# Kernel optimization log

Hardware: AMD Instinct MI355X
Metric: run time of the kernel (lower is better)

Reference implementation:

```python
import jax, jax.numpy as jnp
import numpy as np

B, L, D_IN, H, C = 64, 2048, 400, 200, 32
NEG = 1e12


def setup_inputs() -> dict:
    key = jax.random.key(0)
    k1, k2, k3, k4, k5 = jax.random.split(key, 5)
    x = jax.random.normal(k1, (B, L, D_IN), dtype=jnp.float32)
    category_bias = jax.random.normal(k2, (B, L, C), dtype=jnp.float32)
    att_mask = (jax.random.uniform(k3, (B, L)) > 0.2).astype(jnp.float32)
    # glorot-uniform-ish scales
    W_proj = jax.random.normal(k4, (D_IN, H), dtype=jnp.float32) * np.float32(np.sqrt(2.0 / (D_IN + H)))
    context = jax.random.normal(k5, (C, H), dtype=jnp.float32) * np.float32(np.sqrt(2.0 / (C + H)))
    lamada = jnp.zeros((1,), dtype=jnp.float32)
    return {"x": x, "category_bias": category_bias, "att_mask": att_mask,
            "W_proj": W_proj, "context": context, "lamada": lamada}


def reference(x, category_bias, att_mask, W_proj, context, lamada):
    # proj: [B, L, H] = tanh(x @ W_proj)  (Dense, no bias)
    proj = jnp.tanh(jnp.einsum("bld,dh->blh", x, W_proj))
    # scores vs learned context vectors: [B, L, C]
    weights = jnp.einsum("blh,ch->blc", proj, context) + lamada * category_bias
    # [B, C, L]
    weights = jnp.transpose(weights, (0, 2, 1))
    # additive large-negative mask, then softmax over sequence
    weights = weights - (1.0 - att_mask[:, None, :]) * NEG
    weights = jax.nn.softmax(weights, axis=-1)
    # poly representation: [B, C, D_IN]
    return jnp.einsum("bcl,bld->bcd", weights, x)
```

## Files before the change

### kernel.cpp

```cpp
#include <hip/hip_runtime.h>
#include <cmath>
#include <cstdint>

#define B_ 64
#define L_ 2048
#define DIN 400
#define H_ 200
#define C_ 32
#define NEGBIG 1e12f
#define KC1 13
#define NT1 13
#define KC2 7
#define MT2 2
#define NLC 8

typedef _Float16 half8 __attribute__((ext_vector_type(8)));
typedef float f32x4 __attribute__((ext_vector_type(4)));
typedef unsigned int uint4v __attribute__((ext_vector_type(4)));

__device__ __align__(16) _Float16 g_wfrag[KC1 * NT1 * 512];
__device__ __align__(16) _Float16 g_cfrag[KC2 * MT2 * 512];

static __device__ __forceinline__ f32x4 mfma16(half8 a, half8 b, f32x4 c) {
  return __builtin_amdgcn_mfma_f32_16x16x32_f16(a, b, c, 0, 0, 0);
}

static __device__ __forceinline__ float fast_tanh(float v) {
  const float e = __expf(2.0f * v);
  return 1.0f - 2.0f / (e + 1.0f);
}

__global__ __launch_bounds__(64) void k_prep(const float* __restrict__ Wp,
                                             const float* __restrict__ ctx)
{
  const int lane = threadIdx.x;
  const int bid = blockIdx.x;
  if (bid < KC1 * NT1) {
    const int q = bid / NT1, nt = bid % NT1;
    const int kb = q * 32 + (lane >> 4) * 8;
    const int n  = nt * 16 + (lane & 15);
    half8 h;
#pragma unroll
    for (int j = 0; j < 8; ++j) {
      const int k = kb + j;
      const float v = (k < DIN && n < H_) ? Wp[(size_t)k * H_ + n] : 0.0f;
      h[j] = (_Float16)v;
    }
    *reinterpret_cast<half8*>(&g_wfrag[((size_t)bid << 9) + (lane << 3)]) = h;
  } else {
    const int r = bid - KC1 * NT1;
    const int c  = (r % MT2) * 16 + (lane & 15);
    const int hb = (r / MT2) * 32 + (lane >> 4) * 8;
    half8 h;
#pragma unroll
    for (int j = 0; j < 8; ++j) {
      const int hh = hb + j;
      const float v = (hh < H_) ? ctx[(size_t)c * H_ + hh] : 0.0f;
      h[j] = (_Float16)v;
    }
    *reinterpret_cast<half8*>(&g_cfrag[((size_t)r << 9) + (lane << 3)]) = h;
  }
}

__global__ __launch_bounds__(256, 4) void k_scores(
    const float* __restrict__ x,
    const float* __restrict__ cb,
    const float* __restrict__ mask,
    const float* __restrict__ lam,
    float* __restrict__ S)
{
  __shared__ half8 smemv[1792];

  const int tid  = threadIdx.x;
  const int lane = tid & 63;
  const int w    = __builtin_amdgcn_readfirstlane(tid >> 6);
  const int b    = blockIdx.y;
  const int l0   = blockIdx.x * 64;
  const int oct  = lane >> 4;

  f32x4 acc[NT1];
#pragma unroll
  for (int nt = 0; nt < NT1; ++nt) acc[nt] = f32x4{0.f, 0.f, 0.f, 0.f};

  const float* xrow =
      x + ((size_t)b * L_ + l0 + w * 16 + (lane & 15)) * DIN + oct * 8;

  for (int i = w; i < NT1; i += 4) {
    const _Float16* gp = g_wfrag + (((size_t)i) << 9) + (lane << 3);
    __builtin_amdgcn_global_load_lds(
        (const __attribute__((address_space(1))) void*)gp,
        (__attribute__((address_space(3))) void*)(smemv + i * 64),
        16, 0, 0);
  }
  __builtin_amdgcn_sched_barrier(0);
  float4 cur0 = *reinterpret_cast<const float4*>(xrow);
  float4 cur1 = *reinterpret_cast<const float4*>(xrow + 4);

#pragma unroll
  for (int q = 0; q < KC1; ++q) {
    asm volatile("s_waitcnt vmcnt(2)\n\ts_barrier" ::: "memory");

    float4 nx0 = float4{0.f, 0.f, 0.f, 0.f};
    float4 nx1 = float4{0.f, 0.f, 0.f, 0.f};
    if (q < KC1 - 1) {
      const int nb = ((q + 1) & 1) * 832;
      for (int i = w; i < NT1; i += 4) {
        const _Float16* gp =
            g_wfrag + (((size_t)((q + 1) * NT1 + i)) << 9) + (lane << 3);
        __builtin_amdgcn_global_load_lds(
            (const __attribute__((address_space(1))) void*)gp,
            (__attribute__((address_space(3))) void*)(smemv + nb + i * 64),
            16, 0, 0);
      }
      __builtin_amdgcn_sched_barrier(0);
      const int k0 = (q + 1) * 32 + oct * 8;
      if (k0 + 7 < DIN) {
        nx0 = *reinterpret_cast<const float4*>(xrow + (q + 1) * 32);
        nx1 = *reinterpret_cast<const float4*>(xrow + (q + 1) * 32 + 4);
      }
    }

    float fa[8] = {cur0.x, cur0.y, cur0.z, cur0.w,
                   cur1.x, cur1.y, cur1.z, cur1.w};
    half8 ah;
#pragma unroll
    for (int j = 0; j < 8; ++j) ah[j] = (_Float16)fa[j];

    const int base = (q & 1) * 832;
#pragma unroll
    for (int nt = 0; nt < NT1; ++nt) {
      const half8 bh = smemv[base + nt * 64 + lane];
      acc[nt] = mfma16(ah, bh, acc[nt]);
    }
    cur0 = nx0;
    cur1 = nx1;
  }

  __syncthreads();
  if (lane >= 32) {
    half8 z = {};
    smemv[(24 + w) * 64 + lane] = z;
  }
  _Float16* Pp = reinterpret_cast<_Float16*>(smemv);
#pragma unroll
  for (int nt = 0; nt < NT1; ++nt) {
    const int h   = nt * 16 + (lane & 15);
    const int q2  = h >> 5;
    const int lpw = ((h >> 3) & 3) << 4;
    const int jj  = h & 7;
#pragma unroll
    for (int reg = 0; reg < 4; ++reg) {
      const int t = ((lane >> 4) << 2) + reg;
      const float p = fast_tanh(acc[nt][reg]);
      Pp[(size_t)(((q2 * 4 + w) * 64) + lpw + t) * 8 + jj] = (_Float16)p;
    }
  }

  f32x4 s0 = f32x4{0.f, 0.f, 0.f, 0.f};
  f32x4 s1 = f32x4{0.f, 0.f, 0.f, 0.f};
#pragma unroll
  for (int q2 = 0; q2 < KC2; ++q2) {
    const half8 pb = smemv[(q2 * 4 + w) * 64 + lane];
    const half8 c0 = *reinterpret_cast<const half8*>(
        g_cfrag + (((size_t)(q2 * 2)) << 9) + (lane << 3));
    const half8 c1 = *reinterpret_cast<const half8*>(
        g_cfrag + (((size_t)(q2 * 2 + 1)) << 9) + (lane << 3));
    s0 = mfma16(c0, pb, s0);
    s1 = mfma16(c1, pb, s1);
  }

  const int tok = (w << 4) | (lane & 15);
  const size_t bl = (size_t)b * L_ + l0 + tok;
  const float lamv = lam[0];
  const float mk = (1.0f - mask[bl]) * NEGBIG;
  const int cq = (lane >> 4) << 2;
  const float4 cb0 = *reinterpret_cast<const float4*>(cb + bl * C_ + cq);
  const float4 cb1 = *reinterpret_cast<const float4*>(cb + bl * C_ + 16 + cq);
  float* Sp = S + (size_t)b * C_ * L_ + l0 + tok;
  Sp[(size_t)(cq + 0) * L_] = s0[0] + lamv * cb0.x - mk;
  Sp[(size_t)(cq + 1) * L_] = s0[1] + lamv * cb0.y - mk;
  Sp[(size_t)(cq + 2) * L_] = s0[2] + lamv * cb0.z - mk;
  Sp[(size_t)(cq + 3) * L_] = s0[3] + lamv * cb0.w - mk;
  Sp[(size_t)(16 + cq + 0) * L_] = s1[0] + lamv * cb1.x - mk;
  Sp[(size_t)(16 + cq + 1) * L_] = s1[1] + lamv * cb1.y - mk;
  Sp[(size_t)(16 + cq + 2) * L_] = s1[2] + lamv * cb1.z - mk;
  Sp[(size_t)(16 + cq + 3) * L_] = s1[3] + lamv * cb1.w - mk;
}

__global__ __launch_bounds__(256) void k_softmax(float* __restrict__ S,
                                                 _Float16* __restrict__ wh)
{
  const int row = blockIdx.x;
  float* R = S + (size_t)row * L_;
  const int tid = threadIdx.x;

  float v[8];
  float m = -3.4e38f;
#pragma unroll
  for (int j = 0; j < 8; ++j) {
    v[j] = R[tid + 256 * j];
    m = fmaxf(m, v[j]);
  }
#pragma unroll
  for (int o = 32; o > 0; o >>= 1) m = fmaxf(m, __shfl_xor(m, o));

  __shared__ float red[4];
  const int wid = tid >> 6;
  if ((tid & 63) == 0) red[wid] = m;
  __syncthreads();
  m = fmaxf(fmaxf(red[0], red[1]), fmaxf(red[2], red[3]));
  __syncthreads();

  float s = 0.f;
#pragma unroll
  for (int j = 0; j < 8; ++j) {
    v[j] = __expf(v[j] - m);
    s += v[j];
  }
#pragma unroll
  for (int o = 32; o > 0; o >>= 1) s += __shfl_xor(s, o);
  if ((tid & 63) == 0) red[wid] = s;
  __syncthreads();
  s = red[0] + red[1] + red[2] + red[3];

  const float inv = 1.0f / s;
  if (wh != nullptr) {
    _Float16* whr = wh + (size_t)row * L_;
#pragma unroll
    for (int j = 0; j < 8; ++j)
      whr[tid + 256 * j] = (_Float16)(v[j] * inv);
  } else {
#pragma unroll
    for (int j = 0; j < 8; ++j) R[tid + 256 * j] = v[j] * inv;
  }
}

__global__ __launch_bounds__(512, 4) void k_out_mfma(
    const float* __restrict__ x,
    const _Float16* __restrict__ wh,
    float* __restrict__ part)
{
  __shared__ unsigned int xsw[400 * 20];
  __shared__ unsigned int ws16[32][16];

  const int tid  = threadIdx.x;
  const int lane = tid & 63;
  const int w    = __builtin_amdgcn_readfirstlane(tid >> 6);
  const int b    = blockIdx.y;
  const int kq   = blockIdx.x;
  const int l0b  = kq * (L_ / NLC);

  const int ntile0 = (w < 7) ? w * 3 : 21;
  const int NTW    = (w < 7) ? 3 : 4;

  const int n   = lane & 15;
  const int oct = lane >> 4;

  f32x4 acc[4][2];
#pragma unroll
  for (int i = 0; i < 4; ++i) {
    acc[i][0] = f32x4{0.f, 0.f, 0.f, 0.f};
    acc[i][1] = f32x4{0.f, 0.f, 0.f, 0.f};
  }

  const float* xb = x + ((size_t)b * L_ + l0b) * DIN;
  const unsigned int* whb = reinterpret_cast<const unsigned int*>(
      wh + (size_t)b * C_ * L_ + l0b);

  float4 r0[4], r1[4];
  unsigned int wreg;

#pragma unroll
  for (int s = 0; s < 4; ++s) {
    const int i = s * 512 + tid;
    if (s < 3 || i < 1600) {
      const int lp = i / 100, qd = i - lp * 100;
      const float* src = xb + (size_t)(2 * lp) * DIN + 4 * qd;
      r0[s] = *reinterpret_cast<const float4*>(src);
      r1[s] = *reinterpret_cast<const float4*>(src + DIN);
    }
  }
  wreg = whb[((size_t)(tid >> 4) * L_) / 2 + (tid & 15)];

  const int NCH = (L_ / NLC) / 32;
  for (int ch = 0; ch < NCH; ++ch) {
    __syncthreads();

#pragma unroll
    for (int s = 0; s < 4; ++s) {
      const int i = s * 512 + tid;
      if (s < 3 || i < 1600) {
        const int lp = i / 100, qd = i - lp * 100;
#pragma unroll
        for (int k = 0; k < 4; ++k) {
          const int d = 4 * qd + k;
          const int sw = ((d >> 2) ^ (d >> 4)) & 3;
          const int col = (((lp >> 2) ^ sw) << 2) | (lp & 3);
          const _Float16 h0 = (_Float16)r0[s][k];
          const _Float16 h1 = (_Float16)r1[s][k];
          unsigned int pk = (unsigned int)__builtin_bit_cast(unsigned short, h0) |
                            ((unsigned int)__builtin_bit_cast(unsigned short, h1) << 16);
          xsw[d * 20 + col] = pk;
        }
      }
    }
    ws16[tid >> 4][tid & 15] = wreg;
    __syncthreads();

    if (ch + 1 < NCH) {
      const float* xc = xb + (size_t)((ch + 1) * 32) * DIN;
#pragma unroll
      for (int s = 0; s < 4; ++s) {
        const int i = s * 512 + tid;
        if (s < 3 || i < 1600) {
          const int lp = i / 100, qd = i - lp * 100;
          const float* src = xc + (size_t)(2 * lp) * DIN + 4 * qd;
          r0[s] = *reinterpret_cast<const float4*>(src);
          r1[s] = *reinterpret_cast<const float4*>(src + DIN);
        }
      }
      wreg = whb[((size_t)(tid >> 4) * L_ + (ch + 1) * 32) / 2 + (tid & 15)];
    }

    union { uint4v u; half8 h; } a0c, a1c;
    a0c.u = *reinterpret_cast<const uint4v*>(&ws16[n][oct * 4]);
    a1c.u = *reinterpret_cast<const uint4v*>(&ws16[n + 16][oct * 4]);
    const half8 a0 = a0c.h;
    const half8 a1 = a1c.h;

#pragma unroll
    for (int nt = 0; nt < 4; ++nt) {
      if (nt < NTW) {
        const int d0 = (ntile0 + nt) * 16 + n;
        const int sw = ((d0 >> 2) ^ (d0 >> 4)) & 3;
        const half8 bh = *reinterpret_cast<const half8*>(
            &xsw[d0 * 20 + ((oct ^ sw) << 2)]);
        acc[nt][0] = mfma16(a0, bh, acc[nt][0]);
        acc[nt][1] = mfma16(a1, bh, acc[nt][1]);
      }
    }
  }

  float* pb = part + ((size_t)(b * NLC + kq) * C_) * DIN;
#pragma unroll
  for (int nt = 0; nt < 4; ++nt) {
    if (nt < NTW) {
      const int d = (ntile0 + nt) * 16 + n;
#pragma unroll
      for (int mt = 0; mt < 2; ++mt) {
#pragma unroll
        for (int reg = 0; reg < 4; ++reg) {
          const int c = mt * 16 + oct * 4 + reg;
          pb[(size_t)c * DIN + d] = acc[nt][mt][reg];
        }
      }
    }
  }
}

__global__ __launch_bounds__(256) void k_out_reduce(
    const float* __restrict__ part, float* __restrict__ out)
{
  const int idx = blockIdx.x * 256 + threadIdx.x;
  const int b = idx / (C_ * DIN / 4);
  const int r = idx - b * (C_ * DIN / 4);
  const float4* p = reinterpret_cast<const float4*>(part) +
                    (size_t)b * NLC * (C_ * DIN / 4) + r;
  float4 s = float4{0.f, 0.f, 0.f, 0.f};
#pragma unroll
  for (int lc = 0; lc < NLC; ++lc) {
    const float4 v = p[(size_t)lc * (C_ * DIN / 4)];
    s.x += v.x; s.y += v.y; s.z += v.z; s.w += v.w;
  }
  reinterpret_cast<float4*>(out)[idx] = s;
}

__global__ __launch_bounds__(256) void k_out_atomic(
    const float* __restrict__ x,
    const float* __restrict__ Wt,
    float* __restrict__ out)
{
  __shared__ float ws_s[C_][256];
  const int tid  = threadIdx.x;
  const int b    = blockIdx.y;
  const int lc0  = blockIdx.x * 256;
  const int g    = __builtin_amdgcn_readfirstlane(tid >> 6);
  const int lane = tid & 63;

  {
    const int c  = tid >> 3;
    const int lb = (tid & 7) * 32;
    const float* src = Wt + ((size_t)b * C_ + c) * L_ + lc0 + lb;
#pragma unroll
    for (int j = 0; j < 32; j += 4)
      *reinterpret_cast<float4*>(&ws_s[c][lb + j]) =
          *reinterpret_cast<const float4*>(src + j);
  }
  __syncthreads();

  float a1[8][4] = {};
  float a2[8][4] = {};
  const bool has2 = lane < 36;
  const float* xb = x + ((size_t)b * L_ + lc0) * DIN;
  const int d1 = lane * 4;
  const int d2 = 256 + lane * 4;

  for (int l = 0; l < 256; ++l) {
    const float4 xv = *reinterpret_cast<const float4*>(xb + (size_t)l * DIN + d1);
    float4 xv2 = float4{0.f, 0.f, 0.f, 0.f};
    if (has2) xv2 = *reinterpret_cast<const float4*>(xb + (size_t)l * DIN + d2);
#pragma unroll
    for (int i = 0; i < 8; ++i) {
      const float wv = ws_s[g * 8 + i][l];
      a1[i][0] = fmaf(wv, xv.x, a1[i][0]);
      a1[i][1] = fmaf(wv, xv.y, a1[i][1]);
      a1[i][2] = fmaf(wv, xv.z, a1[i][2]);
      a1[i][3] = fmaf(wv, xv.w, a1[i][3]);
      a2[i][0] = fmaf(wv, xv2.x, a2[i][0]);
      a2[i][1] = fmaf(wv, xv2.y, a2[i][1]);
      a2[i][2] = fmaf(wv, xv2.z, a2[i][2]);
      a2[i][3] = fmaf(wv, xv2.w, a2[i][3]);
    }
  }

  float* ob = out + ((size_t)b * C_ + g * 8) * DIN;
#pragma unroll
  for (int i = 0; i < 8; ++i) {
#pragma unroll
    for (int kk = 0; kk < 4; ++kk)
      atomicAdd(ob + (size_t)i * DIN + d1 + kk, a1[i][kk]);
    if (has2) {
#pragma unroll
      for (int kk = 0; kk < 4; ++kk)
        atomicAdd(ob + (size_t)i * DIN + d2 + kk, a2[i][kk]);
    }
  }
}

extern "C" void kernel_launch(void* const* d_in, const int* in_sizes, int n_in,
                              void* d_out, int out_size, void* d_ws, size_t ws_size,
                              hipStream_t stream)
{
  const float* x    = (const float*)d_in[0];
  const float* cb   = (const float*)d_in[1];
  const float* mask = (const float*)d_in[2];
  const float* Wp   = (const float*)d_in[3];
  const float* ctx  = (const float*)d_in[4];
  const float* lam  = (const float*)d_in[5];
  float* out = (float*)d_out;

  const size_t part_elems = (size_t)B_ * NLC * C_ * DIN;
  float* wsf  = (float*)d_ws;
  float* S    = wsf;
  float* part = wsf;
  _Float16* wh = (_Float16*)(wsf + part_elems);
  const size_t need = part_elems * sizeof(float) +
                      (size_t)B_ * C_ * L_ * sizeof(_Float16);

  k_prep<<<dim3(KC1 * NT1 + KC2 * MT2), 64, 0, stream>>>(Wp, ctx);
  k_scores<<<dim3(L_ / 64, B_), 256, 0, stream>>>(x, cb, mask, lam, S);

  if (ws_size >= need) {
    k_softmax<<<dim3(B_ * C_), 256, 0, stream>>>(S, wh);
    k_out_mfma<<<dim3(NLC, B_), 512, 0, stream>>>(x, wh, part);
    k_out_reduce<<<dim3(B_ * C_ * DIN / 4 / 256), 256, 0, stream>>>(part, out);
  } else {
    k_softmax<<<dim3(B_ * C_), 256, 0, stream>>>(S, nullptr);
    hipMemsetAsync(d_out, 0, (size_t)out_size * sizeof(float), stream);
    k_out_atomic<<<dim3(L_ / 256, B_), 256, 0, stream>>>(x, S, out);
  }
}
```

Before: 107.0 us.

## Switch score projection GEMM to 32x32x16 MFMA with 2x2 wave tiling

Rewrites the projection GEMM in k_scores to use 32x32x16 f16 MFMA. Waves are arranged as 2 M-tiles by 2 N-halves instead of each wave owning 16 rows across all 13 N-tiles. The W fragment layout in k_prep is rebuilt to match, and the tanh write-back into LDS is remapped for the 32x32 accumulator layout. The goal is fewer MFMA issues and fewer LDS B-fragment reads per FLOP. The trade-offs are higher accumulator register use (launch bounds drop from 4 to 3 blocks), an extra barrier, and uneven work between waves (4 vs 3 N-tiles).

```diff
diff --git a/kernel.cpp b/kernel.cpp
--- a/kernel.cpp
+++ b/kernel.cpp
@@ -8,21 +8,26 @@
 #define H_ 200
 #define C_ 32
 #define NEGBIG 1e12f
-#define KC1 13
-#define NT1 13
+#define KI1 13
+#define KT1 26
+#define NW1 7
 #define KC2 7
 #define MT2 2
 #define NLC 8
 
 typedef _Float16 half8 __attribute__((ext_vector_type(8)));
 typedef float f32x4 __attribute__((ext_vector_type(4)));
+typedef float f32x16 __attribute__((ext_vector_type(16)));
 typedef unsigned int uint4v __attribute__((ext_vector_type(4)));
 
-__device__ __align__(16) _Float16 g_wfrag[KC1 * NT1 * 512];
+__device__ __align__(16) _Float16 g_wfrag[KT1 * NW1 * 512];
 __device__ __align__(16) _Float16 g_cfrag[KC2 * MT2 * 512];
 
 static __device__ __forceinline__ f32x4 mfma16(half8 a, half8 b, f32x4 c) {
   return __builtin_amdgcn_mfma_f32_16x16x32_f16(a, b, c, 0, 0, 0);
+}
+static __device__ __forceinline__ f32x16 mfma32(half8 a, half8 b, f32x16 c) {
+  return __builtin_amdgcn_mfma_f32_32x32x16_f16(a, b, c, 0, 0, 0);
 }
 
 static __device__ __forceinline__ float fast_tanh(float v) {
@@ -35,10 +40,10 @@
 {
   const int lane = threadIdx.x;
   const int bid = blockIdx.x;
-  if (bid < KC1 * NT1) {
-    const int q = bid / NT1, nt = bid % NT1;
-    const int kb = q * 32 + (lane >> 4) * 8;
-    const int n  = nt * 16 + (lane & 15);
+  if (bid < KT1 * NW1) {
+    const int kt = bid / NW1, nt = bid % NW1;
+    const int kb = kt * 16 + (lane >> 5) * 8;
+    const int n  = nt * 32 + (lane & 31);
     half8 h;
 #pragma unroll
     for (int j = 0; j < 8; ++j) {
@@ -48,7 +53,7 @@
     }
     *reinterpret_cast<half8*>(&g_wfrag[((size_t)bid << 9) + (lane << 3)]) = h;
   } else {
-    const int r = bid - KC1 * NT1;
+    const int r = bid - KT1 * NW1;
     const int c  = (r % MT2) * 16 + (lane & 15);
     const int hb = (r / MT2) * 32 + (lane >> 4) * 8;
     half8 h;
@@ -62,7 +67,7 @@
   }
 }
 
-__global__ __launch_bounds__(256, 4) void k_scores(
+__global__ __launch_bounds__(256, 3) void k_scores(
     const float* __restrict__ x,
     const float* __restrict__ cb,
     const float* __restrict__ mask,
@@ -74,18 +79,21 @@
   const int tid  = threadIdx.x;
   const int lane = tid & 63;
   const int w    = __builtin_amdgcn_readfirstlane(tid >> 6);
+  const int mtile = w & 1;
+  const int nh    = w >> 1;
+  const int nt0   = nh * 4;
+  const int NTWV  = nh ? 3 : 4;
   const int b    = blockIdx.y;
   const int l0   = blockIdx.x * 64;
-  const int oct  = lane >> 4;
-
-  f32x4 acc[NT1];
-#pragma unroll
-  for (int nt = 0; nt < NT1; ++nt) acc[nt] = f32x4{0.f, 0.f, 0.f, 0.f};
+
+  f32x16 acc[4];
+#pragma unroll
+  for (int i = 0; i < 4; ++i) acc[i] = f32x16{};
 
   const float* xrow =
-      x + ((size_t)b * L_ + l0 + w * 16 + (lane & 15)) * DIN + oct * 8;
-
-  for (int i = w; i < NT1; i += 4) {
+      x + ((size_t)b * L_ + l0 + mtile * 32 + (lane & 31)) * DIN + (lane >> 5) * 8;
+
+  for (int i = w; i < 14; i += 4) {
     const _Float16* gp = g_wfrag + (((size_t)i) << 9) + (lane << 3);
     __builtin_amdgcn_global_load_lds(
         (const __attribute__((address_space(1))) void*)gp,
@@ -93,68 +101,90 @@
         16, 0, 0);
   }
   __builtin_amdgcn_sched_barrier(0);
-  float4 cur0 = *reinterpret_cast<const float4*>(xrow);
-  float4 cur1 = *reinterpret_cast<const float4*>(xrow + 4);
-
-#pragma unroll
-  for (int q = 0; q < KC1; ++q) {
-    asm volatile("s_waitcnt vmcnt(2)\n\ts_barrier" ::: "memory");
-
-    float4 nx0 = float4{0.f, 0.f, 0.f, 0.f};
-    float4 nx1 = float4{0.f, 0.f, 0.f, 0.f};
-    if (q < KC1 - 1) {
-      const int nb = ((q + 1) & 1) * 832;
-      for (int i = w; i < NT1; i += 4) {
+  float4 cur[2][2];
+#pragma unroll
+  for (int s = 0; s < 2; ++s) {
+    cur[s][0] = *reinterpret_cast<const float4*>(xrow + s * 16);
+    cur[s][1] = *reinterpret_cast<const float4*>(xrow + s * 16 + 4);
+  }
+
+#pragma unroll
+  for (int q = 0; q < KI1; ++q) {
+    asm volatile("s_waitcnt vmcnt(4)\n\ts_barrier" ::: "memory");
+
+    float4 nx[2][2];
+#pragma unroll
+    for (int s = 0; s < 2; ++s) {
+      nx[s][0] = float4{0.f, 0.f, 0.f, 0.f};
+      nx[s][1] = float4{0.f, 0.f, 0.f, 0.f};
+    }
+    if (q < KI1 - 1) {
+      const int nb = ((q + 1) & 1) * 896;
+      for (int i = w; i < 14; i += 4) {
         const _Float16* gp =
-            g_wfrag + (((size_t)((q + 1) * NT1 + i)) << 9) + (lane << 3);
+            g_wfrag + (((size_t)(14 * (q + 1) + i)) << 9) + (lane << 3);
         __builtin_amdgcn_global_load_lds(
             (const __attribute__((address_space(1))) void*)gp,
             (__attribute__((address_space(3))) void*)(smemv + nb + i * 64),
             16, 0, 0);
       }
       __builtin_amdgcn_sched_barrier(0);
-      const int k0 = (q + 1) * 32 + oct * 8;
-      if (k0 + 7 < DIN) {
-        nx0 = *reinterpret_cast<const float4*>(xrow + (q + 1) * 32);
-        nx1 = *reinterpret_cast<const float4*>(xrow + (q + 1) * 32 + 4);
-      }
-    }
-
-    float fa[8] = {cur0.x, cur0.y, cur0.z, cur0.w,
-                   cur1.x, cur1.y, cur1.z, cur1.w};
-    half8 ah;
-#pragma unroll
-    for (int j = 0; j < 8; ++j) ah[j] = (_Float16)fa[j];
-
-    const int base = (q & 1) * 832;
-#pragma unroll
-    for (int nt = 0; nt < NT1; ++nt) {
-      const half8 bh = smemv[base + nt * 64 + lane];
-      acc[nt] = mfma16(ah, bh, acc[nt]);
-    }
-    cur0 = nx0;
-    cur1 = nx1;
+#pragma unroll
+      for (int s = 0; s < 2; ++s) {
+        const int k0 = (q + 1) * 32 + s * 16 + (lane >> 5) * 8;
+        if (k0 + 8 <= DIN) {
+          nx[s][0] = *reinterpret_cast<const float4*>(xrow + (q + 1) * 32 + s * 16);
+          nx[s][1] = *reinterpret_cast<const float4*>(xrow + (q + 1) * 32 + s * 16 + 4);
+        }
+      }
+    }
+
+    const int base = (q & 1) * 896;
+#pragma unroll
+    for (int s = 0; s < 2; ++s) {
+      float fa[8] = {cur[s][0].x, cur[s][0].y, cur[s][0].z, cur[s][0].w,
+                     cur[s][1].x, cur[s][1].y, cur[s][1].z, cur[s][1].w};
+      half8 ah;
+#pragma unroll
+      for (int j = 0; j < 8; ++j) ah[j] = (_Float16)fa[j];
+#pragma unroll
+      for (int ntl = 0; ntl < 4; ++ntl) {
+        if (ntl < NTWV) {
+          const half8 bh = smemv[base + (s * 7 + nt0 + ntl) * 64 + lane];
+          acc[ntl] = mfma32(ah, bh, acc[ntl]);
+        }
+      }
+    }
+#pragma unroll
+    for (int s = 0; s < 2; ++s) {
+      cur[s][0] = nx[s][0];
+      cur[s][1] = nx[s][1];
+    }
   }
 
   __syncthreads();
-  if (lane >= 32) {
-    half8 z = {};
-    smemv[(24 + w) * 64 + lane] = z;
-  }
   _Float16* Pp = reinterpret_cast<_Float16*>(smemv);
-#pragma unroll
-  for (int nt = 0; nt < NT1; ++nt) {
-    const int h   = nt * 16 + (lane & 15);
-    const int q2  = h >> 5;
-    const int lpw = ((h >> 3) & 3) << 4;
-    const int jj  = h & 7;
-#pragma unroll
-    for (int reg = 0; reg < 4; ++reg) {
-      const int t = ((lane >> 4) << 2) + reg;
-      const float p = fast_tanh(acc[nt][reg]);
-      Pp[(size_t)(((q2 * 4 + w) * 64) + lpw + t) * 8 + jj] = (_Float16)p;
-    }
-  }
+  {
+    const int oct2 = (lane >> 3) & 3;
+    const int jj   = lane & 7;
+#pragma unroll
+    for (int ntl = 0; ntl < 4; ++ntl) {
+      if (ntl < NTWV) {
+        const int q2 = nt0 + ntl;
+#pragma unroll
+        for (int reg = 0; reg < 16; ++reg) {
+          const int row = (reg & 3) + 8 * (reg >> 2) + 4 * (lane >> 5);
+          const int tok = mtile * 32 + row;
+          const int tile16 = tok >> 4;
+          const int t = tok & 15;
+          const float p = fast_tanh(acc[ntl][reg]);
+          Pp[(size_t)(((q2 * 4 + tile16) * 64) + oct2 * 16 + t) * 8 + jj] =
+              (_Float16)p;
+        }
+      }
+    }
+  }
+  __syncthreads();
 
   f32x4 s0 = f32x4{0.f, 0.f, 0.f, 0.f};
   f32x4 s1 = f32x4{0.f, 0.f, 0.f, 0.f};
@@ -457,7 +487,7 @@
   const size_t need = part_elems * sizeof(float) +
                       (size_t)B_ * C_ * L_ * sizeof(_Float16);
 
-  k_prep<<<dim3(KC1 * NT1 + KC2 * MT2), 64, 0, stream>>>(Wp, ctx);
+  k_prep<<<dim3(KT1 * NW1 + KC2 * MT2), 64, 0, stream>>>(Wp, ctx);
   k_scores<<<dim3(L_ / 64, B_), 256, 0, stream>>>(x, cb, mask, lam, S);
 
   if (ws_size >= need) {
```

Result: slower. 119.9 us (+12.1%).
